# Optimization experiments

Hardware: AMD Instinct MI355X
Metric: run time of the kernel (lower is better)

The kernel has to match this reference:

```python
import jax, jax.numpy as jnp
import numpy as np

N_NODES = 100000
N_EDGES = 1000000
HIDDEN = 64


def gcn_conv(x, src, dst, ew, W, b, n_nodes):
    """PyG GCNConv with normalize=True, add_self_loops=True, given edge weights.

    out[i] = sum_{(j->i)} d_j^{-1/2} * w_ji * d_i^{-1/2} * (x W)[j] + b
    where degrees include self-loops with weight 1.
    """
    loop = jnp.arange(n_nodes)
    src_f = jnp.concatenate([src, loop])
    dst_f = jnp.concatenate([dst, loop])
    ew_f = jnp.concatenate([ew, jnp.ones((n_nodes,), dtype=ew.dtype)])
    # degree at target nodes (sum of incoming edge weights incl. self-loop)
    deg = jax.ops.segment_sum(ew_f, dst_f, num_segments=n_nodes)
    dinv = jnp.where(deg > 0, jax.lax.rsqrt(deg), 0.0)
    norm = dinv[src_f] * ew_f * dinv[dst_f]  # [E + N]
    h = x @ W  # [N, H] dense projection
    msg = h[src_f] * norm[:, None]  # gather + scale
    out = jax.ops.segment_sum(msg, dst_f, num_segments=n_nodes)  # scatter-add
    return out + b


def setup_inputs() -> dict:
    key = jax.random.key(0)
    k = jax.random.split(key, 6)
    x = jax.random.normal(k[0], (N_NODES, HIDDEN), dtype=jnp.float32)
    edge_index = jax.random.randint(k[1], (2, N_EDGES), 0, N_NODES, dtype=jnp.int64 if jax.config.jax_enable_x64 else jnp.int32)
    edge_weight = jax.random.uniform(k[2], (N_EDGES,), dtype=jnp.float32)
    scale = 1.0 / np.sqrt(HIDDEN)
    W1 = jax.random.normal(k[3], (HIDDEN, HIDDEN), dtype=jnp.float32) * scale
    b1 = jnp.zeros((HIDDEN,), dtype=jnp.float32)
    W2 = jax.random.normal(k[4], (HIDDEN, HIDDEN), dtype=jnp.float32) * scale
    b2 = jnp.zeros((HIDDEN,), dtype=jnp.float32)
    return {"x": x, "edge_index": edge_index, "edge_weight": edge_weight,
            "W1": W1, "b1": b1, "W2": W2, "b2": b2}


def reference(x, edge_index, edge_weight, W1, b1, W2, b2):
    src, dst = edge_index[0], edge_index[1]
    n = x.shape[0]
    h = jax.nn.relu(gcn_conv(x, src, dst, edge_weight, W1, b1, n))
    out = gcn_conv(h, src, dst, edge_weight, W2, b2, n)
    return out
```

## Files before the change

### kernel.cpp

```cpp
#include <hip/hip_runtime.h>

#define HID 64
#define NPB 256
#define CAP 3072
#define DFT 512
#define RCAP 6

typedef __attribute__((ext_vector_type(8))) short bf16x8;
typedef __attribute__((ext_vector_type(4))) float f32x4;

__device__ inline float bf2f(unsigned short u) {
  return __uint_as_float((unsigned int)u << 16);
}
__device__ inline unsigned short f2bf(float f) {
  unsigned int u = __float_as_uint(f);
  u += 0x7fff + ((u >> 16) & 1);
  return (unsigned short)(u >> 16);
}
__device__ inline float bfLo(unsigned int u) { return __uint_as_float(u << 16); }
__device__ inline float bfHi(unsigned int u) { return __uint_as_float(u & 0xffff0000u); }

__global__ __launch_bounds__(DFT) void k_bucket1(const int* __restrict__ src,
                                                 const int* __restrict__ dst,
                                                 const float* __restrict__ ew,
                                                 unsigned int* __restrict__ bucketCnt,
                                                 int2* __restrict__ edges,
                                                 int B, int ept, int nE) {
  __shared__ unsigned int hist[512];
  hist[threadIdx.x] = 0;
  __syncthreads();
  int base = blockIdx.x * DFT * ept;
  for (int i = 0; i < ept; ++i) {
    int e = base + i * DFT + threadIdx.x;
    if (e < nE) atomicAdd(&hist[(unsigned)dst[e] >> 8], 1u);
  }
  __syncthreads();
  for (int c = threadIdx.x; c < B; c += DFT) {
    unsigned int h = hist[c];
    unsigned int b = 0;
    if (h) b = atomicAdd(&bucketCnt[c * 16], h);
    hist[c] = (unsigned)(c * CAP) + b;
  }
  __syncthreads();
  for (int i = 0; i < ept; ++i) {
    int e = base + i * DFT + threadIdx.x;
    if (e < nE) {
      int d = dst[e];
      int c = (unsigned)d >> 8;
      int slot = (int)atomicAdd(&hist[c], 1u);
      if (slot < (c + 1) * CAP)
        edges[slot] = make_int2(src[e] | ((d & 255) << 24), __float_as_int(ew[e]));
    }
  }
}

__global__ __launch_bounds__(DFT) void k_degfillG(int2* __restrict__ edges,
                                                  const unsigned int* __restrict__ bucketCnt,
                                                  const float* __restrict__ X,
                                                  const float* __restrict__ W,
                                                  float* __restrict__ dinv,
                                                  int* __restrict__ rowStart,
                                                  unsigned short* __restrict__ Out, int n) {
  __shared__ float deg[NPB];
  __shared__ int cnt[NPB];
  __shared__ int s[NPB];
  if (threadIdx.x < NPB) {
    deg[threadIdx.x] = 1.0f;
    cnt[threadIdx.x] = 0;
  }
  __syncthreads();
  int c = blockIdx.x;
  int i0 = c * CAP;
  int bc = (int)bucketCnt[c * 16];
  if (bc > CAP - 4) bc = CAP - 4;
  int i1 = i0 + bc;
  int2 rec[RCAP];
  int myCnt = 0;
  for (int i = i0 + threadIdx.x; i < i1; i += DFT) {
    int2 r = edges[i];
#pragma unroll
    for (int k = 0; k < RCAP; ++k)
      if (k == myCnt) rec[k] = r;
    myCnt++;
    int l = (unsigned)r.x >> 24;
    atomicAdd(&deg[l], __int_as_float(r.y));
    atomicAdd(&cnt[l], 1);
  }
  __syncthreads();
  int v = 0;
  if (threadIdx.x < NPB) {
    v = cnt[threadIdx.x];
    s[threadIdx.x] = v;
  }
  __syncthreads();
  for (int o = 1; o < NPB; o <<= 1) {
    int t = (threadIdx.x < NPB && threadIdx.x >= (unsigned)o) ? s[threadIdx.x - o] : 0;
    __syncthreads();
    if (threadIdx.x < NPB) s[threadIdx.x] += t;
    __syncthreads();
  }
  if (threadIdx.x < NPB) {
    int rowBase = i0 + s[threadIdx.x] - v;
    float di = rsqrtf(deg[threadIdx.x]);
    int g = c * NPB + threadIdx.x;
    if (g < n) {
      rowStart[g + 1] = i0 + s[threadIdx.x];
      dinv[g] = di;
    }
    cnt[threadIdx.x] = rowBase;
  }
  if (threadIdx.x < 4) edges[i1 + threadIdx.x] = make_int2(0, 0);
  __syncthreads();
  if (threadIdx.x < NPB) deg[threadIdx.x] = rsqrtf(deg[threadIdx.x]);
  __syncthreads();
#pragma unroll
  for (int k = 0; k < RCAP; ++k) {
    if (k < myCnt) {
      int2 r = rec[k];
      int l = (unsigned)r.x >> 24;
      int pos = atomicAdd(&cnt[l], 1);
      float norm = __int_as_float(r.y) * deg[l];
      edges[pos] = make_int2(r.x & 0xFFFFFF, __float_as_int(norm));
    }
  }
  __syncthreads();
  int wv = threadIdx.x >> 6;
  int lane = threadIdx.x & 63;
  int m16 = lane & 15;
  int q = lane >> 4;
  bf16x8 Bb[4][2], Br[4][2];
#pragma unroll
  for (int nt = 0; nt < 4; ++nt)
#pragma unroll
    for (int kh = 0; kh < 2; ++kh) {
      int ncol = nt * 16 + m16;
      int k0 = kh * 32 + q * 8;
#pragma unroll
      for (int j = 0; j < 8; ++j) {
        float w = W[(k0 + j) * HID + ncol];
        unsigned short wb = f2bf(w);
        Bb[nt][kh][j] = (short)wb;
        Br[nt][kh][j] = (short)f2bf(w - bf2f(wb));
      }
    }
#pragma unroll
  for (int sub = 0; sub < 2; ++sub) {
    int slice = sub * 8 + wv;
    int rowBase2 = c * 256 + slice * 16;
    if (rowBase2 >= n) continue;
    int mc = rowBase2 + m16;
    if (mc >= n) mc = n - 1;
    bf16x8 A[2];
    const float* Xp = X + (size_t)mc * HID;
#pragma unroll
    for (int kh = 0; kh < 2; ++kh) {
      f32x4 x0 = *(const f32x4*)(Xp + kh * 32 + q * 8);
      f32x4 x1 = *(const f32x4*)(Xp + kh * 32 + q * 8 + 4);
#pragma unroll
      for (int j = 0; j < 4; ++j) {
        A[kh][j] = (short)f2bf(x0[j]);
        A[kh][4 + j] = (short)f2bf(x1[j]);
      }
    }
    float dv = deg[slice * 16 + m16];
#pragma unroll
    for (int nt = 0; nt < 4; ++nt) {
      f32x4 acc = {0.f, 0.f, 0.f, 0.f};
      acc = __builtin_amdgcn_mfma_f32_16x16x32_bf16(Bb[nt][0], A[0], acc, 0, 0, 0);
      acc = __builtin_amdgcn_mfma_f32_16x16x32_bf16(Bb[nt][1], A[1], acc, 0, 0, 0);
      acc = __builtin_amdgcn_mfma_f32_16x16x32_bf16(Br[nt][0], A[0], acc, 0, 0, 0);
      acc = __builtin_amdgcn_mfma_f32_16x16x32_bf16(Br[nt][1], A[1], acc, 0, 0, 0);
      if (rowBase2 + m16 < n) {
        ushort4 o;
        o.x = f2bf(acc[0] * dv);
        o.y = f2bf(acc[1] * dv);
        o.z = f2bf(acc[2] * dv);
        o.w = f2bf(acc[3] * dv);
        *(ushort4*)(&Out[(size_t)(rowBase2 + m16) * HID + nt * 16 + q * 4]) = o;
      }
    }
  }
}

template <typename TI>
__global__ __launch_bounds__(256) void k_gemmMF(const TI* __restrict__ X,
                                                const float* __restrict__ W,
                                                const float* __restrict__ dinv,
                                                unsigned short* __restrict__ Out,
                                                int n, int nTiles) {
  int wv = threadIdx.x >> 6;
  int lane = threadIdx.x & 63;
  int m16 = lane & 15;
  int q = lane >> 4;
  bf16x8 Bb[4][2], Br[4][2];
#pragma unroll
  for (int nt = 0; nt < 4; ++nt)
#pragma unroll
    for (int kh = 0; kh < 2; ++kh) {
      int ncol = nt * 16 + m16;
      int k0 = kh * 32 + q * 8;
#pragma unroll
      for (int j = 0; j < 8; ++j) {
        float w = W[(k0 + j) * HID + ncol];
        unsigned short wb = f2bf(w);
        Bb[nt][kh][j] = (short)wb;
        Br[nt][kh][j] = (short)f2bf(w - bf2f(wb));
      }
    }
  for (int t = blockIdx.x; t < nTiles; t += gridDim.x) {
    int rowBase = t * 64 + wv * 16;
    if (rowBase >= n) continue;
    int mc = rowBase + m16;
    if (mc >= n) mc = n - 1;
    bf16x8 A[2];
    if (sizeof(TI) == 2) {
      const unsigned short* Xp = (const unsigned short*)X + (size_t)mc * HID;
      A[0] = *(const bf16x8*)(Xp + q * 8);
      A[1] = *(const bf16x8*)(Xp + 32 + q * 8);
    } else {
      const float* Xp = (const float*)X + (size_t)mc * HID;
#pragma unroll
      for (int kh = 0; kh < 2; ++kh) {
        f32x4 x0 = *(const f32x4*)(Xp + kh * 32 + q * 8);
        f32x4 x1 = *(const f32x4*)(Xp + kh * 32 + q * 8 + 4);
#pragma unroll
        for (int j = 0; j < 4; ++j) {
          A[kh][j] = (short)f2bf(x0[j]);
          A[kh][4 + j] = (short)f2bf(x1[j]);
        }
      }
    }
    float dv = dinv[mc];
#pragma unroll
    for (int nt = 0; nt < 4; ++nt) {
      f32x4 acc = {0.f, 0.f, 0.f, 0.f};
      acc = __builtin_amdgcn_mfma_f32_16x16x32_bf16(Bb[nt][0], A[0], acc, 0, 0, 0);
      acc = __builtin_amdgcn_mfma_f32_16x16x32_bf16(Bb[nt][1], A[1], acc, 0, 0, 0);
      acc = __builtin_amdgcn_mfma_f32_16x16x32_bf16(Br[nt][0], A[0], acc, 0, 0, 0);
      acc = __builtin_amdgcn_mfma_f32_16x16x32_bf16(Br[nt][1], A[1], acc, 0, 0, 0);
      if (rowBase + m16 < n) {
        ushort4 o;
        o.x = f2bf(acc[0] * dv);
        o.y = f2bf(acc[1] * dv);
        o.z = f2bf(acc[2] * dv);
        o.w = f2bf(acc[3] * dv);
        *(ushort4*)(&Out[(size_t)(rowBase + m16) * HID + nt * 16 + q * 4]) = o;
      }
    }
  }
}

template <int OUT_BF16>
__global__ __launch_bounds__(256) void k_agg8(const int2* __restrict__ edges,
                                              const int* __restrict__ rowStart,
                                              const float* __restrict__ dinv,
                                              const uint4* __restrict__ H8,
                                              const float* __restrict__ bias,
                                              void* __restrict__ outp, int n) {
  int gwave = (blockIdx.x * 256 + threadIdx.x) >> 6;
  int lane = threadIdx.x & 63;
  int q = lane >> 3;
  int ql = lane & 7;
  int node = gwave * 8 + q;
  if (node >= n) return;
  int e0 = rowStart[node];
  if ((node & 255) == 0) e0 = (node >> 8) * CAP;
  int e1 = rowStart[node + 1];
  float di = dinv[node];
  uint4 su = H8[(size_t)node * 8 + ql];
  float a0 = di * bfLo(su.x), a1 = di * bfHi(su.x);
  float a2 = di * bfLo(su.y), a3 = di * bfHi(su.y);
  float a4 = di * bfLo(su.z), a5 = di * bfHi(su.z);
  float a6 = di * bfLo(su.w), a7 = di * bfHi(su.w);
  for (int base = e0 & ~1; base < e1; base += 4) {
    int4 p0 = *(const int4*)(edges + base);
    int4 p1 = *(const int4*)(edges + base + 2);
    uint4 h0 = H8[(size_t)(unsigned)p0.x * 8u + ql];
    uint4 h1 = H8[(size_t)(unsigned)p0.z * 8u + ql];
    uint4 h2 = H8[(size_t)(unsigned)p1.x * 8u + ql];
    uint4 h3 = H8[(size_t)(unsigned)p1.z * 8u + ql];
    float n0 = (base >= e0) ? __int_as_float(p0.y) : 0.f;
    float n1 = (base + 1 < e1) ? __int_as_float(p0.w) : 0.f;
    float n2 = (base + 2 < e1) ? __int_as_float(p1.y) : 0.f;
    float n3 = (base + 3 < e1) ? __int_as_float(p1.w) : 0.f;
    a0 = fmaf(n0, bfLo(h0.x), a0); a1 = fmaf(n0, bfHi(h0.x), a1);
    a2 = fmaf(n0, bfLo(h0.y), a2); a3 = fmaf(n0, bfHi(h0.y), a3);
    a4 = fmaf(n0, bfLo(h0.z), a4); a5 = fmaf(n0, bfHi(h0.z), a5);
    a6 = fmaf(n0, bfLo(h0.w), a6); a7 = fmaf(n0, bfHi(h0.w), a7);
    a0 = fmaf(n1, bfLo(h1.x), a0); a1 = fmaf(n1, bfHi(h1.x), a1);
    a2 = fmaf(n1, bfLo(h1.y), a2); a3 = fmaf(n1, bfHi(h1.y), a3);
    a4 = fmaf(n1, bfLo(h1.z), a4); a5 = fmaf(n1, bfHi(h1.z), a5);
    a6 = fmaf(n1, bfLo(h1.w), a6); a7 = fmaf(n1, bfHi(h1.w), a7);
    a0 = fmaf(n2, bfLo(h2.x), a0); a1 = fmaf(n2, bfHi(h2.x), a1);
    a2 = fmaf(n2, bfLo(h2.y), a2); a3 = fmaf(n2, bfHi(h2.y), a3);
    a4 = fmaf(n2, bfLo(h2.z), a4); a5 = fmaf(n2, bfHi(h2.z), a5);
    a6 = fmaf(n2, bfLo(h2.w), a6); a7 = fmaf(n2, bfHi(h2.w), a7);
    a0 = fmaf(n3, bfLo(h3.x), a0); a1 = fmaf(n3, bfHi(h3.x), a1);
    a2 = fmaf(n3, bfLo(h3.y), a2); a3 = fmaf(n3, bfHi(h3.y), a3);
    a4 = fmaf(n3, bfLo(h3.z), a4); a5 = fmaf(n3, bfHi(h3.z), a5);
    a6 = fmaf(n3, bfLo(h3.w), a6); a7 = fmaf(n3, bfHi(h3.w), a7);
  }
  float4 bv0 = ((const float4*)bias)[2 * ql];
  float4 bv1 = ((const float4*)bias)[2 * ql + 1];
  a0 += bv0.x; a1 += bv0.y; a2 += bv0.z; a3 += bv0.w;
  a4 += bv1.x; a5 += bv1.y; a6 += bv1.z; a7 += bv1.w;
  if (OUT_BF16) {
    a0 = fmaxf(a0, 0.f); a1 = fmaxf(a1, 0.f); a2 = fmaxf(a2, 0.f); a3 = fmaxf(a3, 0.f);
    a4 = fmaxf(a4, 0.f); a5 = fmaxf(a5, 0.f); a6 = fmaxf(a6, 0.f); a7 = fmaxf(a7, 0.f);
    uint4 o;
    o.x = (unsigned)f2bf(a0) | ((unsigned)f2bf(a1) << 16);
    o.y = (unsigned)f2bf(a2) | ((unsigned)f2bf(a3) << 16);
    o.z = (unsigned)f2bf(a4) | ((unsigned)f2bf(a5) << 16);
    o.w = (unsigned)f2bf(a6) | ((unsigned)f2bf(a7) << 16);
    ((uint4*)outp)[(size_t)node * 8 + ql] = o;
  } else {
    float4 o0, o1;
    o0.x = a0; o0.y = a1; o0.z = a2; o0.w = a3;
    o1.x = a4; o1.y = a5; o1.z = a6; o1.w = a7;
    ((float4*)outp)[(size_t)node * 16 + 2 * ql] = o0;
    ((float4*)outp)[(size_t)node * 16 + 2 * ql + 1] = o1;
  }
}

extern "C" void kernel_launch(void* const* d_in, const int* in_sizes, int n_in,
                              void* d_out, int out_size, void* d_ws, size_t ws_size,
                              hipStream_t stream) {
  const float* x  = (const float*)d_in[0];
  const int*   ei = (const int*)d_in[1];
  const float* ew = (const float*)d_in[2];
  const float* W1 = (const float*)d_in[3];
  const float* b1 = (const float*)d_in[4];
  const float* W2 = (const float*)d_in[5];
  const float* b2 = (const float*)d_in[6];
  float* out = (float*)d_out;

  const int n  = in_sizes[0] / HID;
  const int nE = in_sizes[2];
  const int* src = ei;
  const int* dst = ei + nE;

  const int B = (n + NPB - 1) / NPB;
  const int G1  = (nE + DFT * 4 - 1) / (DFT * 4);
  const int ept = (nE + G1 * DFT - 1) / (G1 * DFT);

  auto align512 = [](size_t v) { return (v + 511) & ~(size_t)511; };
  char* ws = (char*)d_ws;
  size_t off = 0;
  float* dinv        = (float*)(ws + off); off += align512((size_t)n * 4);
  int*   rowStart    = (int*)  (ws + off); off += align512((size_t)(n + 1) * 4);
  unsigned int* bucketCnt = (unsigned int*)(ws + off); off += align512((size_t)B * 16 * 4);
  int2*  edges       = (int2*) (ws + off); off += align512((size_t)B * CAP * 8 + 64);
  unsigned short* bufA = (unsigned short*)(ws + off); off += align512((size_t)n * HID * 2);
  unsigned short* bufB = (unsigned short*)d_out;

  const int aggBlocks = (((n + 7) / 8) * 64 + 255) / 256;
  const int nTiles = (n + 63) / 64;

  hipMemsetAsync(bucketCnt, 0, (size_t)B * 16 * 4, stream);
  k_bucket1<<<G1, DFT, 0, stream>>>(src, dst, ew, bucketCnt, edges, B, ept, nE);
  k_degfillG<<<B, DFT, 0, stream>>>(edges, bucketCnt, x, W1, dinv, rowStart, bufA, n);

  k_agg8<1><<<aggBlocks, 256, 0, stream>>>(edges, rowStart, dinv,
                                           (const uint4*)bufA, b1, bufB, n);

  k_gemmMF<unsigned short><<<1024, 256, 0, stream>>>(bufB, W2, dinv, bufA, n, nTiles);
  k_agg8<0><<<aggBlocks, 256, 0, stream>>>(edges, rowStart, dinv,
                                           (const uint4*)bufA, b2, out, n);
}
```

Measured before the change: 194.0 us.

## Fuse layer-1 aggregation with layer-2 projection GEMM via shared memory

```diff
diff --git a/kernel.cpp b/kernel.cpp
--- a/kernel.cpp
+++ b/kernel.cpp
@@ -182,81 +182,122 @@
   }
 }
 
-template <typename TI>
-__global__ __launch_bounds__(256) void k_gemmMF(const TI* __restrict__ X,
-                                                const float* __restrict__ W,
-                                                const float* __restrict__ dinv,
-                                                unsigned short* __restrict__ Out,
-                                                int n, int nTiles) {
-  int wv = threadIdx.x >> 6;
-  int lane = threadIdx.x & 63;
-  int m16 = lane & 15;
-  int q = lane >> 4;
-  bf16x8 Bb[4][2], Br[4][2];
-#pragma unroll
-  for (int nt = 0; nt < 4; ++nt)
-#pragma unroll
-    for (int kh = 0; kh < 2; ++kh) {
-      int ncol = nt * 16 + m16;
-      int k0 = kh * 32 + q * 8;
-#pragma unroll
-      for (int j = 0; j < 8; ++j) {
-        float w = W[(k0 + j) * HID + ncol];
-        unsigned short wb = f2bf(w);
-        Bb[nt][kh][j] = (short)wb;
-        Br[nt][kh][j] = (short)f2bf(w - bf2f(wb));
-      }
-    }
-  for (int t = blockIdx.x; t < nTiles; t += gridDim.x) {
-    int rowBase = t * 64 + wv * 16;
-    if (rowBase >= n) continue;
-    int mc = rowBase + m16;
-    if (mc >= n) mc = n - 1;
-    bf16x8 A[2];
-    if (sizeof(TI) == 2) {
-      const unsigned short* Xp = (const unsigned short*)X + (size_t)mc * HID;
-      A[0] = *(const bf16x8*)(Xp + q * 8);
-      A[1] = *(const bf16x8*)(Xp + 32 + q * 8);
-    } else {
-      const float* Xp = (const float*)X + (size_t)mc * HID;
-#pragma unroll
-      for (int kh = 0; kh < 2; ++kh) {
-        f32x4 x0 = *(const f32x4*)(Xp + kh * 32 + q * 8);
-        f32x4 x1 = *(const f32x4*)(Xp + kh * 32 + q * 8 + 4);
-#pragma unroll
-        for (int j = 0; j < 4; ++j) {
-          A[kh][j] = (short)f2bf(x0[j]);
-          A[kh][4 + j] = (short)f2bf(x1[j]);
-        }
-      }
-    }
-    float dv = dinv[mc];
-#pragma unroll
-    for (int nt = 0; nt < 4; ++nt) {
-      f32x4 acc = {0.f, 0.f, 0.f, 0.f};
-      acc = __builtin_amdgcn_mfma_f32_16x16x32_bf16(Bb[nt][0], A[0], acc, 0, 0, 0);
-      acc = __builtin_amdgcn_mfma_f32_16x16x32_bf16(Bb[nt][1], A[1], acc, 0, 0, 0);
-      acc = __builtin_amdgcn_mfma_f32_16x16x32_bf16(Br[nt][0], A[0], acc, 0, 0, 0);
-      acc = __builtin_amdgcn_mfma_f32_16x16x32_bf16(Br[nt][1], A[1], acc, 0, 0, 0);
-      if (rowBase + m16 < n) {
-        ushort4 o;
-        o.x = f2bf(acc[0] * dv);
-        o.y = f2bf(acc[1] * dv);
-        o.z = f2bf(acc[2] * dv);
-        o.w = f2bf(acc[3] * dv);
-        *(ushort4*)(&Out[(size_t)(rowBase + m16) * HID + nt * 16 + q * 4]) = o;
-      }
-    }
-  }
-}
-
-template <int OUT_BF16>
-__global__ __launch_bounds__(256) void k_agg8(const int2* __restrict__ edges,
+__global__ __launch_bounds__(256) void k_aggG(const int2* __restrict__ edges,
                                               const int* __restrict__ rowStart,
                                               const float* __restrict__ dinv,
                                               const uint4* __restrict__ H8,
                                               const float* __restrict__ bias,
-                                              void* __restrict__ outp, int n) {
+                                              const float* __restrict__ W,
+                                              unsigned short* __restrict__ Out,
+                                              int n) {
+  __shared__ uint4 sh[32][10];
+  __shared__ float sdi[32];
+  int wv = threadIdx.x >> 6;
+  int lane = threadIdx.x & 63;
+  int q = lane >> 3;
+  int ql = lane & 7;
+  int base = blockIdx.x * 32;
+  int node = base + wv * 8 + q;
+  if (node < n) {
+    int e0 = rowStart[node];
+    if ((node & 255) == 0) e0 = (node >> 8) * CAP;
+    int e1 = rowStart[node + 1];
+    float di = dinv[node];
+    uint4 su = H8[(size_t)node * 8 + ql];
+    float a0 = di * bfLo(su.x), a1 = di * bfHi(su.x);
+    float a2 = di * bfLo(su.y), a3 = di * bfHi(su.y);
+    float a4 = di * bfLo(su.z), a5 = di * bfHi(su.z);
+    float a6 = di * bfLo(su.w), a7 = di * bfHi(su.w);
+    for (int b2 = e0 & ~1; b2 < e1; b2 += 4) {
+      int4 p0 = *(const int4*)(edges + b2);
+      int4 p1 = *(const int4*)(edges + b2 + 2);
+      uint4 h0 = H8[(size_t)(unsigned)p0.x * 8u + ql];
+      uint4 h1 = H8[(size_t)(unsigned)p0.z * 8u + ql];
+      uint4 h2 = H8[(size_t)(unsigned)p1.x * 8u + ql];
+      uint4 h3 = H8[(size_t)(unsigned)p1.z * 8u + ql];
+      float n0 = (b2 >= e0) ? __int_as_float(p0.y) : 0.f;
+      float n1 = (b2 + 1 < e1) ? __int_as_float(p0.w) : 0.f;
+      float n2 = (b2 + 2 < e1) ? __int_as_float(p1.y) : 0.f;
+      float n3 = (b2 + 3 < e1) ? __int_as_float(p1.w) : 0.f;
+      a0 = fmaf(n0, bfLo(h0.x), a0); a1 = fmaf(n0, bfHi(h0.x), a1);
+      a2 = fmaf(n0, bfLo(h0.y), a2); a3 = fmaf(n0, bfHi(h0.y), a3);
+      a4 = fmaf(n0, bfLo(h0.z), a4); a5 = fmaf(n0, bfHi(h0.z), a5);
+      a6 = fmaf(n0, bfLo(h0.w), a6); a7 = fmaf(n0, bfHi(h0.w), a7);
+      a0 = fmaf(n1, bfLo(h1.x), a0); a1 = fmaf(n1, bfHi(h1.x), a1);
+      a2 = fmaf(n1, bfLo(h1.y), a2); a3 = fmaf(n1, bfHi(h1.y), a3);
+      a4 = fmaf(n1, bfLo(h1.z), a4); a5 = fmaf(n1, bfHi(h1.z), a5);
+      a6 = fmaf(n1, bfLo(h1.w), a6); a7 = fmaf(n1, bfHi(h1.w), a7);
+      a0 = fmaf(n2, bfLo(h2.x), a0); a1 = fmaf(n2, bfHi(h2.x), a1);
+      a2 = fmaf(n2, bfLo(h2.y), a2); a3 = fmaf(n2, bfHi(h2.y), a3);
+      a4 = fmaf(n2, bfLo(h2.z), a4); a5 = fmaf(n2, bfHi(h2.z), a5);
+      a6 = fmaf(n2, bfLo(h2.w), a6); a7 = fmaf(n2, bfHi(h2.w), a7);
+      a0 = fmaf(n3, bfLo(h3.x), a0); a1 = fmaf(n3, bfHi(h3.x), a1);
+      a2 = fmaf(n3, bfLo(h3.y), a2); a3 = fmaf(n3, bfHi(h3.y), a3);
+      a4 = fmaf(n3, bfLo(h3.z), a4); a5 = fmaf(n3, bfHi(h3.z), a5);
+      a6 = fmaf(n3, bfLo(h3.w), a6); a7 = fmaf(n3, bfHi(h3.w), a7);
+    }
+    float4 bv0 = ((const float4*)bias)[2 * ql];
+    float4 bv1 = ((const float4*)bias)[2 * ql + 1];
+    a0 = fmaxf(a0 + bv0.x, 0.f); a1 = fmaxf(a1 + bv0.y, 0.f);
+    a2 = fmaxf(a2 + bv0.z, 0.f); a3 = fmaxf(a3 + bv0.w, 0.f);
+    a4 = fmaxf(a4 + bv1.x, 0.f); a5 = fmaxf(a5 + bv1.y, 0.f);
+    a6 = fmaxf(a6 + bv1.z, 0.f); a7 = fmaxf(a7 + bv1.w, 0.f);
+    uint4 o;
+    o.x = (unsigned)f2bf(a0) | ((unsigned)f2bf(a1) << 16);
+    o.y = (unsigned)f2bf(a2) | ((unsigned)f2bf(a3) << 16);
+    o.z = (unsigned)f2bf(a4) | ((unsigned)f2bf(a5) << 16);
+    o.w = (unsigned)f2bf(a6) | ((unsigned)f2bf(a7) << 16);
+    sh[wv * 8 + q][ql] = o;
+    if (ql == 0) sdi[wv * 8 + q] = di;
+  } else {
+    sh[wv * 8 + q][ql] = make_uint4(0, 0, 0, 0);
+    if (ql == 0) sdi[wv * 8 + q] = 0.f;
+  }
+  __syncthreads();
+  int m16 = lane & 15;
+  int qq = lane >> 4;
+  bf16x8 Bb[2], Br[2];
+#pragma unroll
+  for (int kh = 0; kh < 2; ++kh) {
+    int ncol = wv * 16 + m16;
+    int k0 = kh * 32 + qq * 8;
+#pragma unroll
+    for (int j = 0; j < 8; ++j) {
+      float w = W[(k0 + j) * HID + ncol];
+      unsigned short wb = f2bf(w);
+      Bb[kh][j] = (short)wb;
+      Br[kh][j] = (short)f2bf(w - bf2f(wb));
+    }
+  }
+#pragma unroll
+  for (int rt = 0; rt < 2; ++rt) {
+    int row = rt * 16 + m16;
+    bf16x8 A0 = *(const bf16x8*)&sh[row][qq];
+    bf16x8 A1 = *(const bf16x8*)&sh[row][4 + qq];
+    f32x4 acc = {0.f, 0.f, 0.f, 0.f};
+    acc = __builtin_amdgcn_mfma_f32_16x16x32_bf16(Bb[0], A0, acc, 0, 0, 0);
+    acc = __builtin_amdgcn_mfma_f32_16x16x32_bf16(Bb[1], A1, acc, 0, 0, 0);
+    acc = __builtin_amdgcn_mfma_f32_16x16x32_bf16(Br[0], A0, acc, 0, 0, 0);
+    acc = __builtin_amdgcn_mfma_f32_16x16x32_bf16(Br[1], A1, acc, 0, 0, 0);
+    int gnode = base + row;
+    if (gnode < n) {
+      float dv = sdi[row];
+      ushort4 o;
+      o.x = f2bf(acc[0] * dv);
+      o.y = f2bf(acc[1] * dv);
+      o.z = f2bf(acc[2] * dv);
+      o.w = f2bf(acc[3] * dv);
+      *(ushort4*)(&Out[(size_t)gnode * HID + wv * 16 + qq * 4]) = o;
+    }
+  }
+}
+
+__global__ __launch_bounds__(256) void k_agg8f(const int2* __restrict__ edges,
+                                               const int* __restrict__ rowStart,
+                                               const float* __restrict__ dinv,
+                                               const uint4* __restrict__ H8,
+                                               const float* __restrict__ bias,
+                                               float* __restrict__ outp, int n) {
   int gwave = (blockIdx.x * 256 + threadIdx.x) >> 6;
   int lane = threadIdx.x & 63;
   int q = lane >> 3;
@@ -302,24 +343,11 @@
   }
   float4 bv0 = ((const float4*)bias)[2 * ql];
   float4 bv1 = ((const float4*)bias)[2 * ql + 1];
-  a0 += bv0.x; a1 += bv0.y; a2 += bv0.z; a3 += bv0.w;
-  a4 += bv1.x; a5 += bv1.y; a6 += bv1.z; a7 += bv1.w;
-  if (OUT_BF16) {
-    a0 = fmaxf(a0, 0.f); a1 = fmaxf(a1, 0.f); a2 = fmaxf(a2, 0.f); a3 = fmaxf(a3, 0.f);
-    a4 = fmaxf(a4, 0.f); a5 = fmaxf(a5, 0.f); a6 = fmaxf(a6, 0.f); a7 = fmaxf(a7, 0.f);
-    uint4 o;
-    o.x = (unsigned)f2bf(a0) | ((unsigned)f2bf(a1) << 16);
-    o.y = (unsigned)f2bf(a2) | ((unsigned)f2bf(a3) << 16);
-    o.z = (unsigned)f2bf(a4) | ((unsigned)f2bf(a5) << 16);
-    o.w = (unsigned)f2bf(a6) | ((unsigned)f2bf(a7) << 16);
-    ((uint4*)outp)[(size_t)node * 8 + ql] = o;
-  } else {
-    float4 o0, o1;
-    o0.x = a0; o0.y = a1; o0.z = a2; o0.w = a3;
-    o1.x = a4; o1.y = a5; o1.z = a6; o1.w = a7;
-    ((float4*)outp)[(size_t)node * 16 + 2 * ql] = o0;
-    ((float4*)outp)[(size_t)node * 16 + 2 * ql + 1] = o1;
-  }
+  float4 o0, o1;
+  o0.x = a0 + bv0.x; o0.y = a1 + bv0.y; o0.z = a2 + bv0.z; o0.w = a3 + bv0.w;
+  o1.x = a4 + bv1.x; o1.y = a5 + bv1.y; o1.z = a6 + bv1.z; o1.w = a7 + bv1.w;
+  ((float4*)outp)[(size_t)node * 16 + 2 * ql] = o0;
+  ((float4*)outp)[(size_t)node * 16 + 2 * ql + 1] = o1;
 }
 
 extern "C" void kernel_launch(void* const* d_in, const int* in_sizes, int n_in,
@@ -350,20 +378,18 @@
   int*   rowStart    = (int*)  (ws + off); off += align512((size_t)(n + 1) * 4);
   unsigned int* bucketCnt = (unsigned int*)(ws + off); off += align512((size_t)B * 16 * 4);
   int2*  edges       = (int2*) (ws + off); off += align512((size_t)B * CAP * 8 + 64);
-  unsigned short* bufA = (unsigned short*)(ws + off); off += align512((size_t)n * HID * 2);
-  unsigned short* bufB = (unsigned short*)d_out;
-
-  const int aggBlocks = (((n + 7) / 8) * 64 + 255) / 256;
-  const int nTiles = (n + 63) / 64;
+  unsigned short* P2 = (unsigned short*)(ws + off); off += align512((size_t)n * HID * 2);
+  unsigned short* P1 = (unsigned short*)d_out;
+
+  const int aggBlocks = (n + 31) / 32;
 
   hipMemsetAsync(bucketCnt, 0, (size_t)B * 16 * 4, stream);
   k_bucket1<<<G1, DFT, 0, stream>>>(src, dst, ew, bucketCnt, edges, B, ept, nE);
-  k_degfillG<<<B, DFT, 0, stream>>>(edges, bucketCnt, x, W1, dinv, rowStart, bufA, n);
-
-  k_agg8<1><<<aggBlocks, 256, 0, stream>>>(edges, rowStart, dinv,
-                                           (const uint4*)bufA, b1, bufB, n);
-
-  k_gemmMF<unsigned short><<<1024, 256, 0, stream>>>(bufB, W2, dinv, bufA, n, nTiles);
-  k_agg8<0><<<aggBlocks, 256, 0, stream>>>(edges, rowStart, dinv,
-                                           (const uint4*)bufA, b2, out, n);
-}
+  k_degfillG<<<B, DFT, 0, stream>>>(edges, bucketCnt, x, W1, dinv, rowStart, P1, n);
+
+  k_aggG<<<aggBlocks, 256, 0, stream>>>(edges, rowStart, dinv,
+                                        (const uint4*)P1, b1, W2, P2, n);
+
+  k_agg8f<<<aggBlocks, 256, 0, stream>>>(edges, rowStart, dinv,
+                                         (const uint4*)P2, b2, out, n);
+}
```

Result: faster. 182.4 us (-6.0%).
